# Performance work log

Hardware: AMD Instinct MI355X
Metric: run time of the kernel (lower is better)

The kernel has to match this reference:

```python
import jax, jax.numpy as jnp
import numpy as np

RPN_BATCH = 256
ROI_BATCH = 128
IMG = 800.0


def _box_iou(a, b):
    # a: [N,4], b: [G,4] -> [N,G]
    lt = jnp.maximum(a[:, None, :2], b[None, :, :2])
    rb = jnp.minimum(a[:, None, 2:], b[None, :, 2:])
    wh = jnp.clip(rb - lt, 0.0)
    inter = wh[..., 0] * wh[..., 1]
    area_a = (a[:, 2] - a[:, 0]) * (a[:, 3] - a[:, 1])
    area_b = (b[:, 2] - b[:, 0]) * (b[:, 3] - b[:, 1])
    return inter / (area_a[:, None] + area_b[None, :] - inter + 1e-6)


def _encode(a, t):
    wa = a[:, 2] - a[:, 0]
    ha = a[:, 3] - a[:, 1]
    xa = a[:, 0] + 0.5 * wa
    ya = a[:, 1] + 0.5 * ha
    wt = t[:, 2] - t[:, 0]
    ht = t[:, 3] - t[:, 1]
    xt = t[:, 0] + 0.5 * wt
    yt = t[:, 1] + 0.5 * ht
    return jnp.stack(((xt - xa) / wa, (yt - ya) / ha,
                      jnp.log(wt / wa + 1e-6), jnp.log(ht / ha + 1e-6)), axis=1)


def _smooth_l1(x):
    ax = jnp.abs(x)
    return jnp.where(ax < 1.0, 0.5 * x * x, ax - 0.5)


def _rpn_loss_one(scores, deltas, anchors, gt):
    # scores [N,1], deltas [N,4], anchors [N,4], gt [G,4]
    ious = _box_iou(anchors, gt)                 # [N,G]
    max_iou = ious.max(axis=1)
    argmax = ious.argmax(axis=1)
    labels = jnp.full((anchors.shape[0],), -1.0, dtype=scores.dtype)
    labels = jnp.where(max_iou < 0.3, 0.0, labels)
    labels = jnp.where(max_iou > 0.7, 1.0, labels)
    labels = labels.at[jnp.argmax(ious, axis=0)].set(1.0)  # each gt's best anchor is positive
    # deterministic subsampling: keep first K in index order (replaces randperm)
    num_pos = RPN_BATCH // 2
    pos = labels == 1.0
    labels = jnp.where(pos & (jnp.cumsum(pos) > num_pos), -1.0, labels)
    n_pos = jnp.sum(labels == 1.0)
    neg = labels == 0.0
    labels = jnp.where(neg & (jnp.cumsum(neg) > (RPN_BATCH - n_pos)), -1.0, labels)
    mask = (labels != -1.0).astype(scores.dtype)
    logit = scores[:, 0]
    t = jnp.clip(labels, 0.0, 1.0)
    bce = jnp.maximum(logit, 0.0) - logit * t + jnp.log1p(jnp.exp(-jnp.abs(logit)))
    cls = jnp.sum(bce * mask) / jnp.maximum(jnp.sum(mask), 1.0)
    tgt = _encode(anchors, gt[argmax])
    posm = (labels == 1.0).astype(scores.dtype)
    n_posf = jnp.sum(posm)
    reg = jnp.where(n_posf > 0,
                    jnp.sum(_smooth_l1(deltas - tgt) * posm[:, None])
                    / jnp.maximum(n_posf * 4.0, 1.0),
                    0.0)
    return cls + reg


def _det_loss_one(cls_scores, bbox_deltas, proposals, gt, gt_labels):
    # cls_scores [P,C], bbox_deltas [P,4C], proposals [P,4], gt [G,4], gt_labels [G]
    P = proposals.shape[0]
    ious = _box_iou(proposals, gt)
    max_iou = ious.max(axis=1)
    argmax = ious.argmax(axis=1)
    assigned = jnp.where(max_iou >= 0.5, gt_labels[argmax], 0)
    num_pos = ROI_BATCH // 4
    pos = assigned > 0
    pos_rank = jnp.cumsum(pos) - 1
    neg_rank = jnp.cumsum(~pos) - 1
    idx = jnp.arange(P)
    # sort key: first up-to-num_pos positives (index order), then negatives,
    # excess positives pushed to the end -> first ROI_BATCH entries are the sample
    key = jnp.where(pos,
                    jnp.where(pos_rank < num_pos, pos_rank, 2 * P + idx),
                    P + neg_rank)
    sampled = jnp.argsort(key)[:ROI_BATCH]
    t_labels = assigned[sampled]
    matched = gt[argmax[sampled]]
    t_deltas = _encode(proposals[sampled], matched)
    logp = jax.nn.log_softmax(cls_scores[sampled], axis=-1)
    cls = -jnp.mean(jnp.take_along_axis(logp, t_labels[:, None], axis=1)[:, 0])
    pd = bbox_deltas[sampled].reshape(ROI_BATCH, -1, 4)
    preds = pd[jnp.arange(ROI_BATCH), t_labels]  # class-specific deltas
    posm = (t_labels > 0).astype(cls_scores.dtype)
    n_pos = jnp.sum(posm)
    reg = jnp.where(n_pos > 0,
                    jnp.sum(_smooth_l1(preds - t_deltas) * posm[:, None])
                    / jnp.maximum(n_pos * 4.0, 1.0),
                    0.0)
    return cls + reg


def _rand_boxes(k, prefix):
    k1, k2 = jax.random.split(k)
    xy = jax.random.uniform(k1, prefix + (2,)) * (IMG - 130.0)
    wh = jax.random.uniform(k2, prefix + (2,)) * 120.0 + 8.0
    return jnp.concatenate([xy, xy + wh], axis=-1)


def setup_inputs() -> dict:
    B, N, P, G, C = 4, 250000, 1000, 32, 81
    key = jax.random.key(0)
    ks = jax.random.split(key, 8)
    return {
        "rpn_scores": jax.random.normal(ks[0], (B, N, 1), dtype=jnp.float32),
        "rpn_deltas": jax.random.normal(ks[1], (B, N, 4), dtype=jnp.float32) * 0.1,
        "cls_scores": jax.random.normal(ks[2], (B * P, C), dtype=jnp.float32),
        "bbox_deltas": jax.random.normal(ks[3], (B * P, 4 * C), dtype=jnp.float32) * 0.1,
        "anchors": _rand_boxes(ks[4], (N,)),
        "proposals": _rand_boxes(ks[5], (B, P)),
        "gt_boxes": _rand_boxes(ks[6], (B, G)),
        "gt_labels": jax.random.randint(ks[7], (B, G), 1, C, dtype=jnp.int32),
    }


def reference(rpn_scores, rpn_deltas, cls_scores, bbox_deltas,
              anchors, proposals, gt_boxes, gt_labels):
    B, P, _ = proposals.shape
    C = cls_scores.shape[-1]
    cls_b = cls_scores.reshape(B, P, C)
    del_b = bbox_deltas.reshape(B, P, 4 * C)
    rpn = jax.vmap(lambda s, d, g: _rpn_loss_one(s, d, anchors, g))(
        rpn_scores, rpn_deltas, gt_boxes)
    det = jax.vmap(_det_loss_one)(cls_b, del_b, proposals, gt_boxes, gt_labels)
    return jnp.sum(rpn) + jnp.sum(det)
```

## Files before the change

kernel.cpp:

```cpp
#include <hip/hip_runtime.h>
#include <math.h>
#include <stdint.h>

#define B_ 4
#define N_ 250000
#define P_ 1000
#define G_ 32
#define C_ 81
#define RPN_BATCH 256
#define ROI_BATCH 128

#define ABLK 1024
#define NBA ((N_ + ABLK - 1) / ABLK)
#define DETB 4

__device__ __forceinline__ float iou_one(float a0, float a1, float a2, float a3,
                                         float areaA,
                                         float b0, float b1, float b2, float b3) {
    float ltx = fmaxf(a0, b0), lty = fmaxf(a1, b1);
    float rbx = fminf(a2, b2), rby = fminf(a3, b3);
    float w = fmaxf(rbx - ltx, 0.f), h = fmaxf(rby - lty, 0.f);
    float inter = w * h;
    float areaB = (b2 - b0) * (b3 - b1);
    return inter / (areaA + areaB - inter + 1e-6f);
}

__device__ __forceinline__ unsigned long long shfl_xor_u64(unsigned long long v, int m) {
    unsigned lo = (unsigned)v, hi = (unsigned)(v >> 32);
    lo = __shfl_xor(lo, m);
    hi = __shfl_xor(hi, m);
    return ((unsigned long long)hi << 32) | lo;
}

__device__ __forceinline__ float smooth_l1(float x) {
    float ax = fabsf(x);
    return (ax < 1.f) ? 0.5f * x * x : ax - 0.5f;
}

__global__ void __launch_bounds__(512, 8) rpn_assign_det(
        const float* __restrict__ anchors, const float* __restrict__ gt_boxes,
        const int* __restrict__ gt_labels, const float* __restrict__ proposals,
        const float* __restrict__ cls_scores, const float* __restrict__ bbox_deltas,
        int8_t* __restrict__ labels, int* __restrict__ posCnt, int* __restrict__ negCnt,
        unsigned long long* __restrict__ blockBest, float* __restrict__ detPart,
        float* __restrict__ out, int out_size) {
    int b = blockIdx.y, tid = threadIdx.x;
    int lane = tid & 63, wave = tid >> 6;

    if (blockIdx.x >= NBA) {
        int h = blockIdx.x - NBA;
        __shared__ float sgt[G_ * 4];
        __shared__ int sgl[G_];
        __shared__ short sassign[P_];
        __shared__ unsigned char sargm[P_];
        __shared__ int ssamp[ROI_BATCH];
        __shared__ int swd[8];
        __shared__ float sc[8], srg[8];
        if (tid < G_ * 4) sgt[tid] = gt_boxes[b * G_ * 4 + tid];
        if (tid < G_) sgl[tid] = gt_labels[b * G_ + tid];
        __syncthreads();

        int myPos = 0;
        int labj[2];
#pragma unroll
        for (int j = 0; j < 2; ++j) {
            int p = tid * 2 + j;
            int labp = 0, am = 0;
            if (p < P_) {
                float4 A = ((const float4*)proposals)[b * P_ + p];
                float areaA = (A.z - A.x) * (A.w - A.y);
                float best = -1.f;
#pragma unroll 8
                for (int g = 0; g < G_; ++g) {
                    float iou = iou_one(A.x, A.y, A.z, A.w, areaA,
                                        sgt[g * 4], sgt[g * 4 + 1], sgt[g * 4 + 2], sgt[g * 4 + 3]);
                    if (iou > best) { best = iou; am = g; }
                }
                labp = (best >= 0.5f) ? sgl[am] : 0;
                sassign[p] = (short)labp;
                sargm[p] = (unsigned char)am;
                labj[j] = labp;
                myPos += (labp > 0);
            } else {
                labj[j] = -1;
            }
        }

        int inc = myPos;
        for (int off = 1; off < 64; off <<= 1) {
            int v = __shfl_up(inc, off);
            if (lane >= off) inc += v;
        }
        if (lane == 63) swd[wave] = inc;
        __syncthreads();
        int basew = 0, total = 0;
        for (int w = 0; w < 8; ++w) { if (w < wave) basew += swd[w]; total += swd[w]; }
        int pp = basew + inc - myPos;
        int npos_kept = min(total, ROI_BATCH / 4);
        int nneg_total = P_ - total;
#pragma unroll
        for (int j = 0; j < 2; ++j) {
            int p = tid * 2 + j;
            if (labj[j] < 0) break;
            int slot;
            if (labj[j] > 0) {
                slot = (pp < ROI_BATCH / 4) ? pp : npos_kept + nneg_total + (pp - ROI_BATCH / 4);
                pp++;
            } else {
                slot = npos_kept + (p - pp);
            }
            if (slot < ROI_BATCH) ssamp[slot] = p;
        }
        int np_det = npos_kept + max(0, ROI_BATCH - npos_kept - nneg_total);
        __syncthreads();

        int rowBase = h * (ROI_BATCH / DETB) + wave * 4;
        float clsAcc = 0.f;
        for (int k = 0; k < 4; k += 2) {
            int s0 = ssamp[rowBase + k], s1 = ssamp[rowBase + k + 1];
            const float* r0 = cls_scores + ((size_t)(b * P_ + s0)) * C_;
            const float* r1 = cls_scores + ((size_t)(b * P_ + s1)) * C_;
            float a1 = r0[lane], b1 = r1[lane];
            float a2 = (lane < C_ - 64) ? r0[64 + lane] : -INFINITY;
            float b2 = (lane < C_ - 64) ? r1[64 + lane] : -INFINITY;
            float m0 = fmaxf(a1, a2), m1 = fmaxf(b1, b2);
            for (int mm = 32; mm >= 1; mm >>= 1) {
                m0 = fmaxf(m0, __shfl_xor(m0, mm));
                m1 = fmaxf(m1, __shfl_xor(m1, mm));
            }
            float e0 = expf(a1 - m0) + ((lane < C_ - 64) ? expf(a2 - m0) : 0.f);
            float e1 = expf(b1 - m1) + ((lane < C_ - 64) ? expf(b2 - m1) : 0.f);
            for (int mm = 32; mm >= 1; mm >>= 1) {
                e0 += __shfl_xor(e0, mm);
                e1 += __shfl_xor(e1, mm);
            }
            int t0 = sassign[s0], t1 = sassign[s1];
            int q0 = (t0 < 64) ? t0 : t0 - 64;
            int q1 = (t1 < 64) ? t1 : t1 - 64;
            float lo0 = __shfl(a1, q0), hi0 = __shfl(a2, q0);
            float lo1 = __shfl(b1, q1), hi1 = __shfl(b2, q1);
            float v0 = (t0 < 64) ? lo0 : hi0;
            float v1 = (t1 < 64) ? lo1 : hi1;
            if (lane == 0)
                clsAcc += -(v0 - m0 - logf(e0)) - (v1 - m1 - logf(e1));
        }

        float regAcc = 0.f;
        if (lane < 4) {
            int r = rowBase + lane;
            int s = ssamp[r];
            int t = sassign[s];
            if (t > 0) {
                int g = sargm[s];
                float4 A = ((const float4*)proposals)[b * P_ + s];
                float t0g = sgt[g * 4], t1g = sgt[g * 4 + 1];
                float t2g = sgt[g * 4 + 2], t3g = sgt[g * 4 + 3];
                float wa = A.z - A.x, ha = A.w - A.y;
                float xa = A.x + 0.5f * wa, ya = A.y + 0.5f * ha;
                float wt = t2g - t0g, ht = t3g - t1g;
                float xt = t0g + 0.5f * wt, yt = t1g + 0.5f * ht;
                const float4 pd = *(const float4*)(bbox_deltas +
                        ((size_t)(b * P_ + s)) * (4 * C_) + 4 * t);
                regAcc = smooth_l1(pd.x - (xt - xa) / wa) + smooth_l1(pd.y - (yt - ya) / ha) +
                         smooth_l1(pd.z - logf(wt / wa + 1e-6f)) +
                         smooth_l1(pd.w - logf(ht / ha + 1e-6f));
            }
        }
        for (int mm = 32; mm >= 1; mm >>= 1) regAcc += __shfl_xor(regAcc, mm);
        if (lane == 0) { sc[wave] = clsAcc; srg[wave] = regAcc; }
        __syncthreads();
        if (tid == 0) {
            float cp = 0.f, rp = 0.f;
            for (int w = 0; w < 8; ++w) { cp += sc[w]; rp += srg[w]; }
            detPart[b * DETB + h] = cp / (float)ROI_BATCH +
                ((np_det > 0) ? rp / fmaxf((float)np_det * 4.f, 1.f) : 0.f);
        }
        return;
    }

    __shared__ float4 sA[ABLK];
    __shared__ unsigned char sPart[8][ABLK];
    __shared__ int sCnt[16];

    int base = blockIdx.x * ABLK;

    if (blockIdx.x == 0 && b == 0) {
        for (int i = tid; i < out_size; i += 512) out[i] = 0.f;
    }

    for (int t = tid; t < ABLK; t += 512) {
        int ai = base + t;
        float4 v = make_float4(0.f, 0.f, 0.f, 0.f);
        if (ai < N_) v = ((const float4*)anchors)[ai];
        sA[t] = v;
    }
    __syncthreads();

    int waveu = __builtin_amdgcn_readfirstlane(wave);

    const float4* gt4 = (const float4*)gt_boxes + b * G_ + waveu * 4;
    float g0[4], g1[4], g2[4], g3[4], gae[4];
#pragma unroll
    for (int j = 0; j < 4; ++j) {
        float4 g = gt4[j];
        g0[j] = g.x; g1[j] = g.y; g2[j] = g.z; g3[j] = g.w;
        gae[j] = (g.z - g.x) * (g.w - g.y) + 1e-6f;
    }

    float bi[4], bd[4]; int bx[4];
#pragma unroll
    for (int j = 0; j < 4; ++j) { bi[j] = 0.f; bd[j] = 1.f; bx[j] = 0; }

    for (int k = 0; k < ABLK / 64; ++k) {
        int a = k * 64 + lane;
        float4 A = sA[a];
        float areaA = (A.z - A.x) * (A.w - A.y);
        int gidx = base + a;
        float acc03 = 1e30f, acc07 = 1e30f;
#pragma unroll
        for (int j = 0; j < 4; ++j) {
            float ltx = fmaxf(A.x, g0[j]), lty = fmaxf(A.y, g1[j]);
            float rbx = fminf(A.z, g2[j]), rby = fminf(A.w, g3[j]);
            float w = fmaxf(rbx - ltx, 0.f), h = fmaxf(rby - lty, 0.f);
            float inter = w * h;
            float d = (areaA + gae[j]) - inter;
            acc03 = fminf(acc03, fmaf(0.3f, d, -inter));
            acc07 = fminf(acc07, fmaf(0.7f, d, -inter));
            float p1 = inter * bd[j], p2 = bi[j] * d;
            if (p1 > p2) { bi[j] = inter; bd[j] = d; bx[j] = gidx; }
        }
        sPart[wave][a] = (unsigned char)(((acc07 < 0.f) ? 2 : 0) | ((acc03 > 0.f) ? 1 : 0));
    }

#pragma unroll
    for (int j = 0; j < 4; ++j) {
        float i_ = bi[j], d_ = bd[j]; int x_ = bx[j];
        for (int m = 32; m >= 1; m >>= 1) {
            float oi = __shfl_xor(i_, m), od = __shfl_xor(d_, m);
            int ox = __shfl_xor(x_, m);
            float pa = oi * d_, pb = i_ * od;
            bool take = (pa > pb) || (pa == pb && ox < x_);
            if (take) { i_ = oi; d_ = od; x_ = ox; }
        }
        if (lane == 0) {
            float iou = i_ / d_;
            unsigned long long pk =
                (((unsigned long long)__float_as_uint(iou)) << 32) |
                (unsigned)(0xFFFFFFFFu - (unsigned)x_);
            blockBest[((size_t)b * G_ + wave * 4 + j) * NBA + blockIdx.x] = pk;
        }
    }
    __syncthreads();

    int cp = 0, cn = 0;
    if (tid < ABLK / 4) {
        unsigned andb = 0xFFFFFFFFu, orb = 0u;
#pragma unroll
        for (int w = 0; w < 8; ++w) {
            unsigned u = ((const unsigned*)&sPart[w][0])[tid];
            andb &= u; orb |= u;
        }
        int gbase = base + tid * 4;
        unsigned outw = 0;
#pragma unroll
        for (int j = 0; j < 4; ++j) {
            int above = (orb >> (8 * j + 1)) & 1;
            int below = (andb >> (8 * j)) & 1;
            int lab = above ? 1 : (below ? 0 : -1);
            if (gbase + j < N_) { cp += (lab == 1); cn += (lab == 0); }
            outw |= ((unsigned)(unsigned char)(char)lab) << (8 * j);
        }
        if (gbase < N_)
            ((unsigned*)labels)[(((size_t)b * N_ + base) >> 2) + tid] = outw;
    }

    for (int m = 32; m >= 1; m >>= 1) { cp += __shfl_xor(cp, m); cn += __shfl_xor(cn, m); }
    if (lane == 0) { sCnt[wave] = cp; sCnt[8 + wave] = cn; }
    __syncthreads();
    if (tid == 0) {
        int tp = 0, tn = 0;
        for (int w = 0; w < 8; ++w) { tp += sCnt[w]; tn += sCnt[8 + w]; }
        posCnt[b * NBA + blockIdx.x] = tp;
        negCnt[b * NBA + blockIdx.x] = tn;
    }
}

__global__ void __launch_bounds__(256) rpn_sample(
        const int8_t* __restrict__ labels, const float* __restrict__ rpn_scores,
        const float* __restrict__ rpn_deltas, const float* __restrict__ anchors,
        const float* __restrict__ gt_boxes,
        const int* __restrict__ posCnt, const int* __restrict__ negCnt,
        const unsigned long long* __restrict__ blockBest,
        const float* __restrict__ detPart, float* __restrict__ out) {
    int b = blockIdx.y, tid = threadIdx.x;
    int base = blockIdx.x * ABLK;
    int lane = tid & 63, wave = tid >> 6;
    __shared__ float sg[G_ * 4];
    __shared__ int sp[256], sn[256];
    __shared__ unsigned swin[G_];
    __shared__ int sBase[6];
    __shared__ int sWT[8];
    __shared__ int swP[4], swN[4];
    __shared__ float sred[8];

    if (tid < G_ * 4) sg[tid] = gt_boxes[b * G_ * 4 + tid];
    sp[tid] = (tid < NBA) ? posCnt[b * NBA + tid] : 0;
    sn[tid] = (tid < NBA) ? negCnt[b * NBA + tid] : 0;

    {
        int g = tid >> 3, sub = tid & 7;
        unsigned long long v = 0;
        for (int j = sub; j < NBA; j += 8) {
            unsigned long long x = blockBest[((size_t)b * G_ + g) * NBA + j];
            if (x > v) v = x;
        }
        for (int m = 4; m >= 1; m >>= 1) {
            unsigned long long o = shfl_xor_u64(v, m);
            if (o > v) v = o;
        }
        if (sub == 0) swin[g] = 0xFFFFFFFFu - (unsigned)(v & 0xFFFFFFFFull);
    }
    __syncthreads();

    if (tid < G_) {
        unsigned w = swin[tid];
        bool first = true;
        for (int j = 0; j < tid; ++j) if (swin[j] == w) first = false;
        if (first) {
            int8_t old = labels[(size_t)b * N_ + w];
            int blk = (int)(w / ABLK);
            if (old != 1) atomicAdd(&sp[blk], 1);
            if (old == 0) atomicAdd(&sn[blk], -1);
        }
    }
    __syncthreads();

    int vp = sp[tid], vn = sn[tid];
    int ipp = vp, inn2 = vn;
    for (int off = 1; off < 64; off <<= 1) {
        int a = __shfl_up(ipp, off), c = __shfl_up(inn2, off);
        if (lane >= off) { ipp += a; inn2 += c; }
    }
    if (lane == 63) { sWT[wave] = ipp; sWT[4 + wave] = inn2; }
    __syncthreads();
    int preP = 0, preN = 0;
    for (int w = 0; w < wave; ++w) { preP += sWT[w]; preN += sWT[4 + w]; }
    int inclP = preP + ipp, inclN = preN + inn2;
    if (tid == blockIdx.x) {
        sBase[0] = inclP - vp; sBase[1] = inclN - vn;
        sBase[4] = vp; sBase[5] = vn;
    }
    if (tid == 255) { sBase[2] = inclP; sBase[3] = inclN; }
    __syncthreads();

    int posB = sBase[0], negB = sBase[1], totP = sBase[2], totN = sBase[3];
    int cPblk = sBase[4], cNblk = sBase[5];
    int npos = min(totP, RPN_BATCH / 2);
    int negQ = RPN_BATCH - npos;
    bool active = (cPblk > 0 && posB < RPN_BATCH / 2) || (cNblk > 0 && negB < negQ);
    if (!active && blockIdx.x != 0) return;

    int gbase = base + tid * 4;
    unsigned word = 0xFFFFFFFFu;
    if (gbase < N_)
        word = ((const unsigned*)labels)[(((size_t)b * N_ + base) >> 2) + tid];
    int lab[4];
#pragma unroll
    for (int j = 0; j < 4; ++j) lab[j] = (int)(char)((word >> (8 * j)) & 0xFF);
    for (int g = 0; g < G_; ++g) {
        int d = (int)swin[g] - gbase;
        if (d >= 0 && d < 4) lab[d] = 1;
    }
    int cntP = 0, cntN = 0;
#pragma unroll
    for (int j = 0; j < 4; ++j) {
        if (gbase + j < N_) { cntP += (lab[j] == 1); cntN += (lab[j] == 0); }
    }

    int ip = cntP, inn = cntN;
    for (int off = 1; off < 64; off <<= 1) {
        int vpp = __shfl_up(ip, off), vnn = __shfl_up(inn, off);
        if (lane >= off) { ip += vpp; inn += vnn; }
    }
    if (lane == 63) { swP[wave] = ip; swN[wave] = inn; }
    __syncthreads();
    int bP = 0, bN = 0;
    for (int w = 0; w < wave; ++w) { bP += swP[w]; bN += swN[w]; }
    int pP = posB + bP + ip - cntP;
    int pN = negB + bN + inn - cntN;

    float bce = 0.f, regv = 0.f;
#pragma unroll
    for (int j = 0; j < 4; ++j) {
        int i = gbase + j;
        if (i >= N_) break;
        if (lab[j] == 1) {
            int r = pP++;
            if (r < RPN_BATCH / 2) {
                float l = rpn_scores[(size_t)b * N_ + i];
                bce += fmaxf(l, 0.f) - l + log1pf(expf(-fabsf(l)));
                float4 A = ((const float4*)anchors)[i];
                float areaA = (A.z - A.x) * (A.w - A.y);
                float best = -1.f; int am = 0;
                for (int g = 0; g < G_; ++g) {
                    float iou = iou_one(A.x, A.y, A.z, A.w, areaA,
                                        sg[g * 4], sg[g * 4 + 1], sg[g * 4 + 2], sg[g * 4 + 3]);
                    if (iou > best) { best = iou; am = g; }
                }
                float t0 = sg[am * 4], t1 = sg[am * 4 + 1], t2 = sg[am * 4 + 2], t3 = sg[am * 4 + 3];
                float wa = A.z - A.x, ha = A.w - A.y;
                float xa = A.x + 0.5f * wa, ya = A.y + 0.5f * ha;
                float wt = t2 - t0, ht = t3 - t1;
                float xt = t0 + 0.5f * wt, yt = t1 + 0.5f * ht;
                float4 D = ((const float4*)rpn_deltas)[(size_t)b * N_ + i];
                regv += smooth_l1(D.x - (xt - xa) / wa) + smooth_l1(D.y - (yt - ya) / ha) +
                        smooth_l1(D.z - logf(wt / wa + 1e-6f)) + smooth_l1(D.w - logf(ht / ha + 1e-6f));
            }
        } else if (lab[j] == 0) {
            int r = pN++;
            if (r < negQ) {
                float l = rpn_scores[(size_t)b * N_ + i];
                bce += fmaxf(l, 0.f) + log1pf(expf(-fabsf(l)));
            }
        }
    }
    for (int m = 32; m >= 1; m >>= 1) { bce += __shfl_xor(bce, m); regv += __shfl_xor(regv, m); }
    if (lane == 0) { sred[wave] = bce; sred[4 + wave] = regv; }
    __syncthreads();
    if (tid == 0) {
        float sb = sred[0] + sred[1] + sred[2] + sred[3];
        float sr = sred[4] + sred[5] + sred[6] + sred[7];
        int rnp = min(totP, RPN_BATCH / 2);
        int kneg = min(totN, RPN_BATCH - rnp);
        float denomC = fmaxf((float)(rnp + kneg), 1.f);
        float contrib = sb / denomC +
                        ((rnp > 0) ? sr / fmaxf((float)rnp * 4.f, 1.f) : 0.f);
        if (blockIdx.x == 0)
            contrib += detPart[b * DETB + 0] + detPart[b * DETB + 1] +
                       detPart[b * DETB + 2] + detPart[b * DETB + 3];
        if (contrib != 0.f || blockIdx.x == 0) atomicAdd(out, contrib);
    }
}

extern "C" void kernel_launch(void* const* d_in, const int* in_sizes, int n_in,
                              void* d_out, int out_size, void* d_ws, size_t ws_size,
                              hipStream_t stream) {
    const float* rpn_scores  = (const float*)d_in[0];
    const float* rpn_deltas  = (const float*)d_in[1];
    const float* cls_scores  = (const float*)d_in[2];
    const float* bbox_deltas = (const float*)d_in[3];
    const float* anchors     = (const float*)d_in[4];
    const float* proposals   = (const float*)d_in[5];
    const float* gt_boxes    = (const float*)d_in[6];
    const int*   gt_labels   = (const int*)d_in[7];
    float* out = (float*)d_out;

    char* ws = (char*)d_ws;
    size_t off = 0;
    auto alloc = [&](size_t bytes) -> char* {
        size_t o = (off + 255) & ~(size_t)255;
        off = o + bytes;
        return ws + o;
    };
    int8_t* labels = (int8_t*)alloc((size_t)B_ * N_);
    int* posCnt = (int*)alloc((size_t)B_ * NBA * 4);
    int* negCnt = (int*)alloc((size_t)B_ * NBA * 4);
    unsigned long long* blockBest = (unsigned long long*)alloc((size_t)B_ * G_ * NBA * 8);
    float* detPart = (float*)alloc(B_ * DETB * 4);

    rpn_assign_det<<<dim3(NBA + DETB, B_), 512, 0, stream>>>(
            anchors, gt_boxes, gt_labels, proposals, cls_scores, bbox_deltas,
            labels, posCnt, negCnt, blockBest, detPart, out, out_size);
    rpn_sample<<<dim3(NBA, B_), 256, 0, stream>>>(labels, rpn_scores, rpn_deltas,
                                                  anchors, gt_boxes, posCnt, negCnt,
                                                  blockBest, detPart, out);
}
```

Before: 137.5 us.

## Compute per-image scan and GT winners once in last-block epilogue

Adds a ticket counter so the last anchor block per image in the assign kernel reduces blockBest, fixes the forced-positive counts, scans pos/neg counts and writes per-block bases, totals, winner indices and active flags. The sample kernel then reads these precomputed values and exits early on inactive blocks. Before, every one of its roughly thousand blocks redid the same reduction and scan. The cost is a serialized epilogue on one block per image, extra threadfences, and an added memset launch.

```diff
diff --git a/kernel.cpp b/kernel.cpp
--- a/kernel.cpp
+++ b/kernel.cpp
@@ -43,6 +43,9 @@
         const float* __restrict__ cls_scores, const float* __restrict__ bbox_deltas,
         int8_t* __restrict__ labels, int* __restrict__ posCnt, int* __restrict__ negCnt,
         unsigned long long* __restrict__ blockBest, float* __restrict__ detPart,
+        int* __restrict__ ticket, int* __restrict__ posBase, int* __restrict__ negBase,
+        int* __restrict__ activeFlag, unsigned* __restrict__ swinOut,
+        int* __restrict__ totPos, int* __restrict__ totNeg,
         float* __restrict__ out, int out_size) {
     int b = blockIdx.y, tid = threadIdx.x;
     int lane = tid & 63, wave = tid >> 6;
@@ -283,82 +286,113 @@
         posCnt[b * NBA + blockIdx.x] = tp;
         negCnt[b * NBA + blockIdx.x] = tn;
     }
+
+    __shared__ int sEpi;
+    __threadfence();
+    __syncthreads();
+    if (tid == 0) sEpi = (atomicAdd(&ticket[b], 1) == NBA - 1) ? 1 : 0;
+    __syncthreads();
+    if (!sEpi) return;
+    __threadfence();
+
+    __shared__ int esp[256], esn[256];
+    __shared__ unsigned eswin[G_];
+    __shared__ int eWTp[4], eWTn[4];
+    __shared__ int sTot[2];
+
+    if (tid < 256) {
+        esp[tid] = (tid < NBA) ? posCnt[b * NBA + tid] : 0;
+        esn[tid] = (tid < NBA) ? negCnt[b * NBA + tid] : 0;
+    }
+    {
+        int g = tid >> 4, sub = tid & 15;
+        unsigned long long v = 0;
+        for (int j = sub; j < NBA; j += 16) {
+            unsigned long long x = blockBest[((size_t)b * G_ + g) * NBA + j];
+            if (x > v) v = x;
+        }
+        for (int m = 8; m >= 1; m >>= 1) {
+            unsigned long long o = shfl_xor_u64(v, m);
+            if (o > v) v = o;
+        }
+        if (sub == 0) {
+            unsigned w = 0xFFFFFFFFu - (unsigned)(v & 0xFFFFFFFFull);
+            eswin[g] = w;
+            swinOut[b * G_ + g] = w;
+        }
+    }
+    __syncthreads();
+    if (tid < G_) {
+        unsigned w = eswin[tid];
+        bool first = true;
+        for (int j = 0; j < tid; ++j) if (eswin[j] == w) first = false;
+        if (first) {
+            int8_t old = labels[(size_t)b * N_ + w];
+            int blk = (int)(w / ABLK);
+            if (old != 1) atomicAdd(&esp[blk], 1);
+            if (old == 0) atomicAdd(&esn[blk], -1);
+        }
+    }
+    __syncthreads();
+    int evp = 0, evn = 0;
+    if (tid < 256) { evp = esp[tid]; evn = esn[tid]; }
+    int eip = evp, ein = evn;
+    for (int off = 1; off < 64; off <<= 1) {
+        int a2 = __shfl_up(eip, off), c2 = __shfl_up(ein, off);
+        if (lane >= off) { eip += a2; ein += c2; }
+    }
+    if (tid < 256 && lane == 63) { eWTp[wave] = eip; eWTn[wave] = ein; }
+    __syncthreads();
+    int exP = 0, exN = 0;
+    if (tid < 256) {
+        int preP = 0, preN = 0;
+        for (int w = 0; w < wave; ++w) { preP += eWTp[w]; preN += eWTn[w]; }
+        int inclP = preP + eip, inclN = preN + ein;
+        exP = inclP - evp; exN = inclN - evn;
+        if (tid < NBA) {
+            posBase[b * NBA + tid] = exP;
+            negBase[b * NBA + tid] = exN;
+        }
+        if (tid == 255) {
+            sTot[0] = inclP; sTot[1] = inclN;
+            totPos[b] = inclP; totNeg[b] = inclN;
+        }
+    }
+    __syncthreads();
+    if (tid < NBA) {
+        int npos = min(sTot[0], RPN_BATCH / 2);
+        int negQ = RPN_BATCH - npos;
+        int act = ((evp > 0 && exP < RPN_BATCH / 2) ||
+                   (evn > 0 && exN < negQ) || tid == 0) ? 1 : 0;
+        activeFlag[b * NBA + tid] = act;
+    }
 }
 
 __global__ void __launch_bounds__(256) rpn_sample(
         const int8_t* __restrict__ labels, const float* __restrict__ rpn_scores,
         const float* __restrict__ rpn_deltas, const float* __restrict__ anchors,
         const float* __restrict__ gt_boxes,
-        const int* __restrict__ posCnt, const int* __restrict__ negCnt,
-        const unsigned long long* __restrict__ blockBest,
+        const int* __restrict__ posBase, const int* __restrict__ negBase,
+        const int* __restrict__ totPos, const int* __restrict__ totNeg,
+        const unsigned* __restrict__ swinIn, const int* __restrict__ activeFlag,
         const float* __restrict__ detPart, float* __restrict__ out) {
     int b = blockIdx.y, tid = threadIdx.x;
+    if (!activeFlag[b * NBA + blockIdx.x]) return;
     int base = blockIdx.x * ABLK;
     int lane = tid & 63, wave = tid >> 6;
     __shared__ float sg[G_ * 4];
-    __shared__ int sp[256], sn[256];
     __shared__ unsigned swin[G_];
-    __shared__ int sBase[6];
-    __shared__ int sWT[8];
     __shared__ int swP[4], swN[4];
     __shared__ float sred[8];
 
     if (tid < G_ * 4) sg[tid] = gt_boxes[b * G_ * 4 + tid];
-    sp[tid] = (tid < NBA) ? posCnt[b * NBA + tid] : 0;
-    sn[tid] = (tid < NBA) ? negCnt[b * NBA + tid] : 0;
-
-    {
-        int g = tid >> 3, sub = tid & 7;
-        unsigned long long v = 0;
-        for (int j = sub; j < NBA; j += 8) {
-            unsigned long long x = blockBest[((size_t)b * G_ + g) * NBA + j];
-            if (x > v) v = x;
-        }
-        for (int m = 4; m >= 1; m >>= 1) {
-            unsigned long long o = shfl_xor_u64(v, m);
-            if (o > v) v = o;
-        }
-        if (sub == 0) swin[g] = 0xFFFFFFFFu - (unsigned)(v & 0xFFFFFFFFull);
-    }
-    __syncthreads();
-
-    if (tid < G_) {
-        unsigned w = swin[tid];
-        bool first = true;
-        for (int j = 0; j < tid; ++j) if (swin[j] == w) first = false;
-        if (first) {
-            int8_t old = labels[(size_t)b * N_ + w];
-            int blk = (int)(w / ABLK);
-            if (old != 1) atomicAdd(&sp[blk], 1);
-            if (old == 0) atomicAdd(&sn[blk], -1);
-        }
-    }
-    __syncthreads();
-
-    int vp = sp[tid], vn = sn[tid];
-    int ipp = vp, inn2 = vn;
-    for (int off = 1; off < 64; off <<= 1) {
-        int a = __shfl_up(ipp, off), c = __shfl_up(inn2, off);
-        if (lane >= off) { ipp += a; inn2 += c; }
-    }
-    if (lane == 63) { sWT[wave] = ipp; sWT[4 + wave] = inn2; }
-    __syncthreads();
-    int preP = 0, preN = 0;
-    for (int w = 0; w < wave; ++w) { preP += sWT[w]; preN += sWT[4 + w]; }
-    int inclP = preP + ipp, inclN = preN + inn2;
-    if (tid == blockIdx.x) {
-        sBase[0] = inclP - vp; sBase[1] = inclN - vn;
-        sBase[4] = vp; sBase[5] = vn;
-    }
-    if (tid == 255) { sBase[2] = inclP; sBase[3] = inclN; }
-    __syncthreads();
-
-    int posB = sBase[0], negB = sBase[1], totP = sBase[2], totN = sBase[3];
-    int cPblk = sBase[4], cNblk = sBase[5];
+    if (tid < G_) swin[tid] = swinIn[b * G_ + tid];
+    int totP = totPos[b];
+    int posB = posBase[b * NBA + blockIdx.x];
+    int negB = negBase[b * NBA + blockIdx.x];
     int npos = min(totP, RPN_BATCH / 2);
     int negQ = RPN_BATCH - npos;
-    bool active = (cPblk > 0 && posB < RPN_BATCH / 2) || (cNblk > 0 && negB < negQ);
-    if (!active && blockIdx.x != 0) return;
+    __syncthreads();
 
     int gbase = base + tid * 4;
     unsigned word = 0xFFFFFFFFu;
@@ -430,8 +464,8 @@
     if (tid == 0) {
         float sb = sred[0] + sred[1] + sred[2] + sred[3];
         float sr = sred[4] + sred[5] + sred[6] + sred[7];
-        int rnp = min(totP, RPN_BATCH / 2);
-        int kneg = min(totN, RPN_BATCH - rnp);
+        int rnp = npos;
+        int kneg = min(totNeg[b], negQ);
         float denomC = fmaxf((float)(rnp + kneg), 1.f);
         float contrib = sb / denomC +
                         ((rnp > 0) ? sr / fmaxf((float)rnp * 4.f, 1.f) : 0.f);
@@ -467,11 +501,22 @@
     int* negCnt = (int*)alloc((size_t)B_ * NBA * 4);
     unsigned long long* blockBest = (unsigned long long*)alloc((size_t)B_ * G_ * NBA * 8);
     float* detPart = (float*)alloc(B_ * DETB * 4);
-
+    int* ticket = (int*)alloc(B_ * 4);
+    int* posBase = (int*)alloc((size_t)B_ * NBA * 4);
+    int* negBase = (int*)alloc((size_t)B_ * NBA * 4);
+    int* activeFlag = (int*)alloc((size_t)B_ * NBA * 4);
+    unsigned* swinOut = (unsigned*)alloc(B_ * G_ * 4);
+    int* totPos = (int*)alloc(B_ * 4);
+    int* totNeg = (int*)alloc(B_ * 4);
+
+    hipMemsetAsync(ticket, 0, B_ * 4, stream);
     rpn_assign_det<<<dim3(NBA + DETB, B_), 512, 0, stream>>>(
             anchors, gt_boxes, gt_labels, proposals, cls_scores, bbox_deltas,
-            labels, posCnt, negCnt, blockBest, detPart, out, out_size);
+            labels, posCnt, negCnt, blockBest, detPart,
+            ticket, posBase, negBase, activeFlag, swinOut, totPos, totNeg,
+            out, out_size);
     rpn_sample<<<dim3(NBA, B_), 256, 0, stream>>>(labels, rpn_scores, rpn_deltas,
-                                                  anchors, gt_boxes, posCnt, negCnt,
-                                                  blockBest, detPart, out);
+                                                  anchors, gt_boxes, posBase, negBase,
+                                                  totPos, totNeg, swinOut, activeFlag,
+                                                  detPart, out);
 }
```

Result: slower. 251.4 us (+82.7%).
